# Kernel tuning notes

Measured on AMD Instinct MI355X. Metric: run time of the kernel, lower is better.

The kernel has to match this reference:

```python
import jax, jax.numpy as jnp
from jax import lax
import numpy as np

MAXLEN, B, D = 2048, 64, 256
CONV_CH = 512

def setup_inputs() -> dict:
    key = jax.random.key(0)
    ks = jax.random.split(key, 10)
    inp = {
        "ctx_val": jax.random.normal(ks[0], (MAXLEN, B, D), jnp.float32),
        "ctx_key": jax.random.normal(ks[1], (MAXLEN, B, D), jnp.float32),
        "ctx_mask": jnp.ones((MAXLEN, B), jnp.float32),
        "attention_past": jax.random.uniform(ks[2], (B, 1, MAXLEN), jnp.float32),
        "ht_query": jax.random.normal(ks[3], (B, D), jnp.float32),
        # learned parameters (torch default inits approximated with scaled normals)
        "W_conv": jax.random.normal(ks[4], (CONV_CH, 1, 3), jnp.float32) * (1.0 / np.sqrt(3.0)),
        "W_query": jax.random.normal(ks[5], (D, D), jnp.float32) * (1.0 / np.sqrt(D)),
        "W_att_past": jax.random.normal(ks[6], (D, CONV_CH), jnp.float32) * (1.0 / np.sqrt(CONV_CH)),
        "b_att_past": jax.random.normal(ks[7], (D,), jnp.float32) * 0.01,
        "W_attn": jax.random.normal(ks[8], (1, D), jnp.float32) * (1.0 / np.sqrt(D)),
        "b_attn": jax.random.normal(ks[9], (1,), jnp.float32) * 0.01,
    }
    return inp

def reference(ctx_val, ctx_key, ctx_mask, attention_past, ht_query,
              W_conv, W_query, W_att_past, b_att_past, W_attn, b_attn):
    # fc_query: (b, D)
    hq = ht_query @ W_query.T
    # conv1d(1->512, k=3, pad=1, no bias): (b, 512, L)
    ap = lax.conv_general_dilated(attention_past, W_conv, window_strides=(1,),
                                  padding=[(1, 1)],
                                  dimension_numbers=("NCH", "OIH", "NCH"))
    # permute(2,0,1) -> (L, b, 512), then fc_att_past -> (L, b, D)
    ap = jnp.einsum("blc,dc->lbd", jnp.transpose(ap, (2, 0, 1)).transpose(1, 0, 2), W_att_past) + b_att_past
    # additive attention score: (L, b)
    s = jnp.tanh(ctx_key + hq[None, :, :] + ap)
    score = jnp.einsum("lbd,d->lb", s, W_attn[0]) + b_attn[0]
    # hard threshold mask, normalize over seq dim
    hard = (score >= 0).astype(jnp.float32) * ctx_mask
    hard = hard / (hard.sum(axis=0) + 1e-10)
    # masked weighted sum over seq dim: (b, D)
    ct = jnp.einsum("lbd,lb->bd", ctx_val, hard)
    return (ct, hard)
```

## Files before the change

### kernel.cpp

```cpp
#include <hip/hip_runtime.h>
#include <math.h>

#define L_MAX 2048
#define BATCH 64
#define DIM   256
#define CCH   512
#define ROWSTRIDE (BATCH * DIM)

#define HQ_OFF   0
#define WF_OFF   16384
#define SUMS_OFF 17152
#define HARD_OFF 19200
#define PART_OFF 150272
#define SUMS_STRIDE 32

__device__ __forceinline__ float fast_tanh(float x) {
    float ax = fabsf(x);
    float e  = __expf(2.0f * ax);
    float r  = 1.0f - 2.0f * __builtin_amdgcn_rcpf(e + 1.0f);
    return copysignf(r, x);
}

__device__ __forceinline__ void gload16(const float* g, float* l) {
    __builtin_amdgcn_global_load_lds(
        (const __attribute__((address_space(1))) void*)g,
        (__attribute__((address_space(3))) void*)l,
        16, 0, 0);
}

__global__ __launch_bounds__(256) void prep_kernel(
    const float* __restrict__ ht_query, const float* __restrict__ W_query,
    const float* __restrict__ W_conv,   const float* __restrict__ W_att_past,
    float* __restrict__ hq, float* __restrict__ wf, float* __restrict__ sums) {
    int t   = threadIdx.x;
    int blk = blockIdx.x;
    if (blk == 0 && t < BATCH) sums[t * SUMS_STRIDE] = 0.f;
    __shared__ float q[DIM];
    if (blk < BATCH) {
        q[t] = ht_query[blk * DIM + t];
        __syncthreads();
        const float4* wrow = (const float4*)(W_query + t * DIM);
        float acc = 0.f;
        #pragma unroll 8
        for (int k = 0; k < DIM / 4; k++) {
            float4 wv = wrow[k];
            acc += q[4*k] * wv.x + q[4*k+1] * wv.y + q[4*k+2] * wv.z + q[4*k+3] * wv.w;
        }
        hq[blk * DIM + t] = acc;
    } else {
        int j = blk - BATCH;
        const float4* wrow = (const float4*)(W_att_past + t * CCH);
        float acc = 0.f;
        #pragma unroll 8
        for (int c = 0; c < CCH / 4; c++) {
            float4 wv = wrow[c];
            acc += W_conv[(4*c  ) * 3 + j] * wv.x + W_conv[(4*c+1) * 3 + j] * wv.y
                 + W_conv[(4*c+2) * 3 + j] * wv.z + W_conv[(4*c+3) * 3 + j] * wv.w;
        }
        wf[j * DIM + t] = acc;
    }
}

__global__ __launch_bounds__(256) void fused_kernel(
    const float* __restrict__ ctx_key, const float* __restrict__ ctx_val,
    const float* __restrict__ ctx_mask, const float* __restrict__ att_past,
    const float* __restrict__ hq, const float* __restrict__ wf,
    const float* __restrict__ b_att_past, const float* __restrict__ W_attn,
    const float* __restrict__ b_attn,
    float* __restrict__ hard_raw, float* __restrict__ sums,
    float* __restrict__ part) {
    __shared__ float kbuf[16 * DIM];
    __shared__ float vbuf[16 * DIM];
    __shared__ float red[4 * DIM];
    __shared__ float c4[4];

    int b     = blockIdx.x & 63;
    int chunk = blockIdx.x >> 6;
    int w     = threadIdx.x >> 6;
    int lane  = threadIdx.x & 63;
    int d0    = lane << 2;
    int l0w   = chunk * 64 + w * 16;

    float4 hq4 = *(const float4*)(hq + b * DIM + d0);
    float4 bp  = *(const float4*)(b_att_past + d0);
    hq4.x += bp.x; hq4.y += bp.y; hq4.z += bp.z; hq4.w += bp.w;
    float4 w0  = *(const float4*)(wf + d0);
    float4 w1  = *(const float4*)(wf + DIM + d0);
    float4 w2  = *(const float4*)(wf + 2 * DIM + d0);
    float4 wa  = *(const float4*)(W_attn + d0);
    float battn = b_attn[0];
    const float* apb = att_past + b * L_MAX;

    float ap[18];
    {
        float4 t0 = *(const float4*)(apb + l0w);
        float4 t1 = *(const float4*)(apb + l0w + 4);
        float4 t2 = *(const float4*)(apb + l0w + 8);
        float4 t3 = *(const float4*)(apb + l0w + 12);
        ap[1]=t0.x; ap[2]=t0.y; ap[3]=t0.z; ap[4]=t0.w;
        ap[5]=t1.x; ap[6]=t1.y; ap[7]=t1.z; ap[8]=t1.w;
        ap[9]=t2.x; ap[10]=t2.y; ap[11]=t2.z; ap[12]=t2.w;
        ap[13]=t3.x; ap[14]=t3.y; ap[15]=t3.z; ap[16]=t3.w;
        ap[0]  = (l0w > 0)          ? apb[l0w - 1]  : 0.f;
        ap[17] = (l0w + 16 < L_MAX) ? apb[l0w + 16] : 0.f;
    }

    float m16[16];
    #pragma unroll
    for (int j = 0; j < 16; j++)
        m16[j] = ctx_mask[(l0w + j) * BATCH + b];

    #pragma unroll
    for (int j = 0; j < 4; j++)
        gload16(ctx_key + (size_t)((l0w + j) * BATCH + b) * DIM + d0,
                &kbuf[(w * 4 + j) * DIM]);
    __syncthreads();

    float h16[16];
    float cnt = 0.f;
    float4 acc = make_float4(0.f, 0.f, 0.f, 0.f);

    #pragma unroll
    for (int s = 0; s < 4; s++) {
        float p[4];
        #pragma unroll
        for (int j = 0; j < 4; j++) {
            int r = 4 * s + j;
            float4 k = *(const float4*)&kbuf[(w * 4 + j) * DIM + d0];
            float am = ap[r], a0 = ap[r + 1], a1 = ap[r + 2];
            float x0 = k.x + hq4.x + am * w0.x + a0 * w1.x + a1 * w2.x;
            float x1 = k.y + hq4.y + am * w0.y + a0 * w1.y + a1 * w2.y;
            float x2 = k.z + hq4.z + am * w0.z + a0 * w1.z + a1 * w2.z;
            float x3 = k.w + hq4.w + am * w0.w + a0 * w1.w + a1 * w2.w;
            p[j] = fast_tanh(x0) * wa.x + fast_tanh(x1) * wa.y +
                   fast_tanh(x2) * wa.z + fast_tanh(x3) * wa.w;
        }
        #pragma unroll
        for (int off = 32; off > 0; off >>= 1) {
            #pragma unroll
            for (int j = 0; j < 4; j++)
                p[j] += __shfl_xor(p[j], off, 64);
        }
        #pragma unroll
        for (int j = 0; j < 4; j++) {
            h16[4 * s + j] = (p[j] + battn >= 0.f) ? m16[4 * s + j] : 0.f;
            cnt += h16[4 * s + j];
        }

        #pragma unroll
        for (int j = 0; j < 4; j++) {
            if (h16[4 * s + j] != 0.f)
                gload16(ctx_val + (size_t)((l0w + 4 * s + j) * BATCH + b) * DIM + d0,
                        &vbuf[(w * 4 + j) * DIM]);
        }
        if (s < 3) {
            #pragma unroll
            for (int j = 0; j < 4; j++)
                gload16(ctx_key + (size_t)((l0w + 4 * (s + 1) + j) * BATCH + b) * DIM + d0,
                        &kbuf[(w * 4 + j) * DIM]);
        }
        __syncthreads();

        #pragma unroll
        for (int j = 0; j < 4; j++) {
            float hv = h16[4 * s + j];
            if (hv != 0.f) {
                float4 v = *(const float4*)&vbuf[(w * 4 + j) * DIM + d0];
                acc.x += v.x * hv; acc.y += v.y * hv;
                acc.z += v.z * hv; acc.w += v.w * hv;
            }
        }
    }

    if (lane == 0) {
        #pragma unroll
        for (int j = 0; j < 16; j++)
            hard_raw[(l0w + j) * BATCH + b] = h16[j];
    }

    *(float4*)(red + w * DIM + d0) = acc;
    if (lane == 0) c4[w] = cnt;
    __syncthreads();
    int d = threadIdx.x;
    float sred = red[d] + red[DIM + d] + red[2 * DIM + d] + red[3 * DIM + d];
    part[(size_t)(chunk * BATCH + b) * DIM + d] = sred;
    if (threadIdx.x == 0)
        atomicAdd(&sums[b * SUMS_STRIDE], c4[0] + c4[1] + c4[2] + c4[3]);
}

__global__ __launch_bounds__(256) void tail_kernel(
    const float* __restrict__ part, const float* __restrict__ hard_raw,
    const float* __restrict__ sums,
    float* __restrict__ ct, float* __restrict__ out_hard) {
    if (blockIdx.x < BATCH) {
        int b = blockIdx.x;
        int d = threadIdx.x;
        float s = 0.f;
        #pragma unroll 8
        for (int c = 0; c < 32; c++)
            s += part[(size_t)(c * BATCH + b) * DIM + d];
        float invZ = 1.0f / (sums[b * SUMS_STRIDE] + 1e-10f);
        ct[b * DIM + d] = s * invZ;
    } else {
        int i = (blockIdx.x - BATCH) * 256 + threadIdx.x;
        float4 h = *(const float4*)(hard_raw + (size_t)i * 4);
        int b0 = (i * 4) & 63;
        float4 o;
        o.x = h.x / (sums[(b0 + 0) * SUMS_STRIDE] + 1e-10f);
        o.y = h.y / (sums[(b0 + 1) * SUMS_STRIDE] + 1e-10f);
        o.z = h.z / (sums[(b0 + 2) * SUMS_STRIDE] + 1e-10f);
        o.w = h.w / (sums[(b0 + 3) * SUMS_STRIDE] + 1e-10f);
        *(float4*)(out_hard + (size_t)i * 4) = o;
    }
}

extern "C" void kernel_launch(void* const* d_in, const int* in_sizes, int n_in,
                              void* d_out, int out_size, void* d_ws, size_t ws_size,
                              hipStream_t stream) {
    const float* ctx_val    = (const float*)d_in[0];
    const float* ctx_key    = (const float*)d_in[1];
    const float* ctx_mask   = (const float*)d_in[2];
    const float* att_past   = (const float*)d_in[3];
    const float* ht_query   = (const float*)d_in[4];
    const float* W_conv     = (const float*)d_in[5];
    const float* W_query    = (const float*)d_in[6];
    const float* W_att_past = (const float*)d_in[7];
    const float* b_att_past = (const float*)d_in[8];
    const float* W_attn     = (const float*)d_in[9];
    const float* b_attn     = (const float*)d_in[10];

    float* ws   = (float*)d_ws;
    float* hq   = ws + HQ_OFF;
    float* wf   = ws + WF_OFF;
    float* sums = ws + SUMS_OFF;
    float* hard = ws + HARD_OFF;
    float* part = ws + PART_OFF;

    float* out_ct   = (float*)d_out;
    float* out_hard = (float*)d_out + BATCH * DIM;

    prep_kernel<<<BATCH + 3, 256, 0, stream>>>(
        ht_query, W_query, W_conv, W_att_past, hq, wf, sums);

    fused_kernel<<<BATCH * 32, 256, 0, stream>>>(
        ctx_key, ctx_val, ctx_mask, att_past, hq, wf, b_att_past, W_attn, b_attn,
        hard, sums, part);

    tail_kernel<<<BATCH + 128, 256, 0, stream>>>(part, hard, sums, out_ct, out_hard);
}
```

Baseline: 322.4 us.

## Double-buffer per-wave key/value loads and drop block-wide barriers

Replaces the block-synchronized key staging and conditional value loads with a per-wave double-buffered LDS pipeline. Each wave issues key and value rows for the next group ahead and waits with vmcnt counters instead of __syncthreads. This is meant to overlap memory latency with the tanh/score computation. In exchange it loads every value row unconditionally, so it no longer skips value traffic for rows with zero hard weight.

```diff
diff --git a/kernel.cpp b/kernel.cpp
--- a/kernel.cpp
+++ b/kernel.cpp
@@ -6,6 +6,7 @@
 #define DIM   256
 #define CCH   512
 #define ROWSTRIDE (BATCH * DIM)
+#define GRP   4
 
 #define HQ_OFF   0
 #define WF_OFF   16384
@@ -69,8 +70,7 @@
     const float* __restrict__ b_attn,
     float* __restrict__ hard_raw, float* __restrict__ sums,
     float* __restrict__ part) {
-    __shared__ float kbuf[16 * DIM];
-    __shared__ float vbuf[16 * DIM];
+    __shared__ __align__(16) float stage[4 * 2 * 2 * GRP * DIM];
     __shared__ float red[4 * DIM];
     __shared__ float c4[4];
 
@@ -80,6 +80,8 @@
     int lane  = threadIdx.x & 63;
     int d0    = lane << 2;
     int l0w   = chunk * 64 + w * 16;
+
+    float* wstage = stage + w * (2 * 2 * GRP * DIM);
 
     float4 hq4 = *(const float4*)(hq + b * DIM + d0);
     float4 bp  = *(const float4*)(b_att_past + d0);
@@ -110,67 +112,68 @@
     for (int j = 0; j < 16; j++)
         m16[j] = ctx_mask[(l0w + j) * BATCH + b];
 
-    #pragma unroll
-    for (int j = 0; j < 4; j++)
-        gload16(ctx_key + (size_t)((l0w + j) * BATCH + b) * DIM + d0,
-                &kbuf[(w * 4 + j) * DIM]);
-    __syncthreads();
+    asm volatile("s_waitcnt vmcnt(0)" ::: "memory");
 
     float h16[16];
     float cnt = 0.f;
     float4 acc = make_float4(0.f, 0.f, 0.f, 0.f);
 
-    #pragma unroll
-    for (int s = 0; s < 4; s++) {
-        float p[4];
-        #pragma unroll
-        for (int j = 0; j < 4; j++) {
-            int r = 4 * s + j;
-            float4 k = *(const float4*)&kbuf[(w * 4 + j) * DIM + d0];
-            float am = ap[r], a0 = ap[r + 1], a1 = ap[r + 2];
-            float x0 = k.x + hq4.x + am * w0.x + a0 * w1.x + a1 * w2.x;
-            float x1 = k.y + hq4.y + am * w0.y + a0 * w1.y + a1 * w2.y;
-            float x2 = k.z + hq4.z + am * w0.z + a0 * w1.z + a1 * w2.z;
-            float x3 = k.w + hq4.w + am * w0.w + a0 * w1.w + a1 * w2.w;
-            p[j] = fast_tanh(x0) * wa.x + fast_tanh(x1) * wa.y +
-                   fast_tanh(x2) * wa.z + fast_tanh(x3) * wa.w;
-        }
-        #pragma unroll
-        for (int off = 32; off > 0; off >>= 1) {
-            #pragma unroll
-            for (int j = 0; j < 4; j++)
-                p[j] += __shfl_xor(p[j], off, 64);
-        }
-        #pragma unroll
-        for (int j = 0; j < 4; j++) {
-            h16[4 * s + j] = (p[j] + battn >= 0.f) ? m16[4 * s + j] : 0.f;
-            cnt += h16[4 * s + j];
-        }
-
-        #pragma unroll
-        for (int j = 0; j < 4; j++) {
-            if (h16[4 * s + j] != 0.f)
-                gload16(ctx_val + (size_t)((l0w + 4 * s + j) * BATCH + b) * DIM + d0,
-                        &vbuf[(w * 4 + j) * DIM]);
-        }
-        if (s < 3) {
-            #pragma unroll
-            for (int j = 0; j < 4; j++)
-                gload16(ctx_key + (size_t)((l0w + 4 * (s + 1) + j) * BATCH + b) * DIM + d0,
-                        &kbuf[(w * 4 + j) * DIM]);
-        }
-        __syncthreads();
-
-        #pragma unroll
-        for (int j = 0; j < 4; j++) {
-            float hv = h16[4 * s + j];
-            if (hv != 0.f) {
-                float4 v = *(const float4*)&vbuf[(w * 4 + j) * DIM + d0];
-                acc.x += v.x * hv; acc.y += v.y * hv;
-                acc.z += v.z * hv; acc.w += v.w * hv;
-            }
-        }
-    }
+    #define ISSUE(g) do {                                                      \
+        float* buf_ = wstage + ((g) & 1) * (2 * GRP * DIM);                    \
+        _Pragma("unroll")                                                      \
+        for (int j = 0; j < GRP; j++)                                          \
+            gload16(ctx_key + (size_t)((l0w + (g) * GRP + j) * BATCH + b) * DIM + d0, \
+                    buf_ + j * DIM);                                           \
+        _Pragma("unroll")                                                      \
+        for (int j = 0; j < GRP; j++)                                          \
+            gload16(ctx_val + (size_t)((l0w + (g) * GRP + j) * BATCH + b) * DIM + d0, \
+                    buf_ + (GRP + j) * DIM);                                   \
+    } while (0)
+
+    #define STEP(g, WAITSTR) do {                                              \
+        asm volatile("s_waitcnt " WAITSTR ::: "memory");                       \
+        __builtin_amdgcn_sched_barrier(0);                                     \
+        const float* buf_ = wstage + ((g) & 1) * (2 * GRP * DIM);              \
+        float p[GRP];                                                          \
+        _Pragma("unroll")                                                      \
+        for (int j = 0; j < GRP; j++) {                                        \
+            int r = (g) * GRP + j;                                             \
+            float4 k = *(const float4*)(buf_ + j * DIM + d0);                  \
+            float am = ap[r], a0 = ap[r + 1], a1 = ap[r + 2];                  \
+            float x0 = k.x + hq4.x + am * w0.x + a0 * w1.x + a1 * w2.x;        \
+            float x1 = k.y + hq4.y + am * w0.y + a0 * w1.y + a1 * w2.y;        \
+            float x2 = k.z + hq4.z + am * w0.z + a0 * w1.z + a1 * w2.z;        \
+            float x3 = k.w + hq4.w + am * w0.w + a0 * w1.w + a1 * w2.w;        \
+            p[j] = fast_tanh(x0) * wa.x + fast_tanh(x1) * wa.y +               \
+                   fast_tanh(x2) * wa.z + fast_tanh(x3) * wa.w;                \
+        }                                                                      \
+        _Pragma("unroll")                                                      \
+        for (int off = 32; off > 0; off >>= 1) {                               \
+            _Pragma("unroll")                                                  \
+            for (int j = 0; j < GRP; j++)                                      \
+                p[j] += __shfl_xor(p[j], off, 64);                             \
+        }                                                                      \
+        _Pragma("unroll")                                                      \
+        for (int j = 0; j < GRP; j++) {                                        \
+            int r = (g) * GRP + j;                                             \
+            float hv = (p[j] + battn >= 0.f) ? m16[r] : 0.f;                   \
+            h16[r] = hv; cnt += hv;                                            \
+            float4 v = *(const float4*)(buf_ + (GRP + j) * DIM + d0);          \
+            acc.x += v.x * hv; acc.y += v.y * hv;                              \
+            acc.z += v.z * hv; acc.w += v.w * hv;                              \
+        }                                                                      \
+        if ((g) < 2) ISSUE((g) + 2);                                           \
+    } while (0)
+
+    ISSUE(0);
+    ISSUE(1);
+    STEP(0, "vmcnt(8)");
+    STEP(1, "vmcnt(8)");
+    STEP(2, "vmcnt(8)");
+    STEP(3, "vmcnt(0)");
+
+    #undef STEP
+    #undef ISSUE
 
     if (lane == 0) {
         #pragma unroll
```

Result: slower. 328.9 us (+2.0%).
